# Performance work log

Hardware: AMD Instinct MI355X
Metric: run time of the kernel (lower is better)

## Reference

```python
import jax, jax.numpy as jnp
import numpy as np

B, BITS, HID = 4096, 64, 512
EPS = 1e-5
TEMPERATURE = 1.0  # buffer default


def _w(k, shape):
    return jax.random.normal(k, shape, jnp.float32) * 0.02


def setup_inputs() -> dict:
    key = jax.random.key(0)
    ks = jax.random.split(key, 8)
    return {
        "a_bits": jax.random.uniform(ks[0], (B, BITS), jnp.float32),
        "shift_bits": jax.random.uniform(ks[1], (B, BITS), jnp.float32),
        # shift_decoder params
        "W1": _w(ks[2], (HID, BITS)), "b1": jnp.zeros((HID,), jnp.float32),
        "g1": jnp.ones((HID,), jnp.float32), "be1": jnp.zeros((HID,), jnp.float32),
        "W2": _w(ks[3], (HID, HID)), "b2": jnp.zeros((HID,), jnp.float32),
        "g2": jnp.ones((HID,), jnp.float32), "be2": jnp.zeros((HID,), jnp.float32),
        "W3": _w(ks[4], (BITS, HID)), "b3": jnp.zeros((BITS,), jnp.float32),
        # index_net params (input dim = 2*BITS)
        "Wi1": _w(ks[5], (HID, 2 * BITS)), "bi1": jnp.zeros((HID,), jnp.float32),
        "Wi2": _w(ks[6], (HID, HID)), "bi2": jnp.zeros((HID,), jnp.float32),
        "Wi3": _w(ks[7], (BITS, HID)), "bi3": jnp.zeros((BITS,), jnp.float32),
    }


def _layernorm(x, g, b):
    m = jnp.mean(x, axis=-1, keepdims=True)
    v = jnp.mean(jnp.square(x - m), axis=-1, keepdims=True)
    return (x - m) * jax.lax.rsqrt(v + EPS) * g + b


def reference(a_bits, shift_bits, W1, b1, g1, be1, W2, b2, g2, be2, W3, b3,
              Wi1, bi1, Wi2, bi2, Wi3, bi3):
    # shift decoder: Linear -> LN -> ReLU -> Linear -> LN -> ReLU -> Linear
    h = jax.nn.relu(_layernorm(shift_bits @ W1.T + b1, g1, be1))
    h = jax.nn.relu(_layernorm(h @ W2.T + b2, g2, be2))
    shift_logits = h @ W3.T + b3                        # [B, BITS]
    shift_soft = jax.nn.softmax(shift_logits / TEMPERATURE, axis=-1)

    # index_net, vectorized over the output-position loop.
    # combined = [one_hot(i), shift_soft]; the one-hot part of the first Linear
    # just selects column i of Wi1[:, :BITS], so we add it as a [BITS, HID] bias.
    pos_part = Wi1[:, :BITS].T                          # [BITS, HID]
    shift_part = shift_soft @ Wi1[:, BITS:].T           # [B, HID]
    h1 = jax.nn.relu(pos_part[None, :, :] + shift_part[:, None, :] + bi1)  # [B, BITS, HID]
    h2 = jax.nn.relu(jnp.einsum('bph,kh->bpk', h1, Wi2) + bi2)             # [B, BITS, HID]
    idx_logits = jnp.einsum('bph,kh->bpk', h2, Wi3) + bi3                  # [B, BITS, BITS]
    idx_soft = jax.nn.softmax(idx_logits / TEMPERATURE, axis=-1)

    # softmax-weighted gather-sum over a_bits
    return jnp.einsum('bpj,bj->bp', idx_soft, a_bits)   # [B, BITS]
```

## Files before the change

kernel.cpp:

```cpp
#include <hip/hip_runtime.h>
#include <hip/hip_bf16.h>
#include <math.h>

#define B_N 4096
#define BITSN 64
#define HID 512
#define EPSV 1e-5f
#define BT 16

typedef unsigned short ushort_t;
typedef __attribute__((ext_vector_type(8))) short bf16x8;
typedef __attribute__((ext_vector_type(4))) float f32x4;
typedef __attribute__((ext_vector_type(16))) float f32x16;

__device__ __forceinline__ ushort_t f2bf(float f) {
  unsigned u = __float_as_uint(f);
  u += 0x7FFF + ((u >> 16) & 1);
  return (ushort_t)(u >> 16);
}

__device__ __forceinline__ unsigned pack2bf(float lo, float hi) {
  union { __hip_bfloat162 h; unsigned u; } cv;
  cv.h = __float22bfloat162_rn(make_float2(lo, hi));
  return cv.u;
}

__device__ __forceinline__ float bf2f(short v) {
  return __uint_as_float(((unsigned)(unsigned short)v) << 16);
}

__global__ __launch_bounds__(256) void prep_kernel(
    const float* __restrict__ Wi2, const float* __restrict__ Wi3,
    const float* __restrict__ Wi1, const float* __restrict__ W1,
    const float* __restrict__ W2, const float* __restrict__ W3,
    ushort_t* __restrict__ Wi1posTb, ushort_t* __restrict__ W1b,
    ushort_t* __restrict__ W2f, ushort_t* __restrict__ W3b,
    ushort_t* __restrict__ Wi1sb, ushort_t* __restrict__ Wi2f32,
    ushort_t* __restrict__ Wi3g) {
  int idx = blockIdx.x * 256 + threadIdx.x;
  if (idx < 512 * 512) {
    {
      int j = idx & 7, lane = (idx >> 3) & 63;
      int ct = (idx >> 9) & 31, ks = idx >> 14;
      int c = ct * 16 + (lane & 15);
      int k = ks * 32 + (lane >> 4) * 8 + j;
      W2f[idx] = f2bf(W2[c * 512 + k]);
    }
    {
      int j = idx & 7, lane = (idx >> 3) & 63;
      int ct = (idx >> 9) & 15, ks = idx >> 13;
      int c = ct * 32 + (lane & 31);
      int k = ks * 16 + (lane >> 5) * 8 + j;
      Wi2f32[idx] = f2bf(Wi2[c * 512 + k]);
    }
  }
  if (idx < 64 * 512) {
    W3b[idx] = f2bf(W3[idx]);
    int p = idx >> 9, i = idx & 511;
    Wi1posTb[idx] = f2bf(Wi1[i * 128 + p]);
    int e = idx & 7, lane = (idx >> 3) & 63;
    int jt = (idx >> 9) & 1, h = (idx >> 10) & 1;
    int mc = (idx >> 11) & 1, w = idx >> 12;
    int jr = jt * 32 + (lane & 31);
    int c = w * 64 + mc * 32 + 16 * h + 4 * (lane >> 5) + (e & 3) + 8 * (e >> 2);
    Wi3g[idx] = f2bf(Wi3[jr * 512 + c]);
  }
  if (idx < 512 * 64) {
    W1b[idx] = f2bf(W1[idx]);
    int j = idx >> 6, k = idx & 63;
    Wi1sb[idx] = f2bf(Wi1[j * 128 + 64 + k]);
  }
}

__global__ __launch_bounds__(256) void shift2_kernel(
    const float* __restrict__ shift_bits,
    const ushort_t* __restrict__ W1b, const float* __restrict__ b1,
    const float* __restrict__ g1, const float* __restrict__ be1,
    const ushort_t* __restrict__ W2f, const float* __restrict__ b2,
    const float* __restrict__ g2, const float* __restrict__ be2,
    const ushort_t* __restrict__ W3b, const float* __restrict__ b3,
    const ushort_t* __restrict__ Wi1sb, const float* __restrict__ bi1,
    float* __restrict__ sp) {
  __shared__ __align__(16) ushort_t hA[BT * 512];
  __shared__ __align__(16) char reg2[32 * 1024];
  __shared__ float b1s[512], g1s[512], be1s[512];
  __shared__ float b2s[512], g2s[512], be2s[512], bi1s[512];
  __shared__ float red[4][BT][2];
  __shared__ float b3s[64];

  ushort_t* sbt = (ushort_t*)reg2;
  ushort_t* h2  = (ushort_t*)reg2;
  float (*lg32)[68] = (float(*)[68])(reg2 + 16 * 1024);
  ushort_t* sb2 = (ushort_t*)(reg2 + 16 * 1024 + 16 * 68 * 4);

  int b0 = blockIdx.x * BT;
  int t = threadIdx.x, w = t >> 6, l = t & 63, lg = l >> 4, l15 = l & 15;

  b1s[t] = b1[t];  b1s[t + 256] = b1[t + 256];
  g1s[t] = g1[t];  g1s[t + 256] = g1[t + 256];
  be1s[t] = be1[t]; be1s[t + 256] = be1[t + 256];
  b2s[t] = b2[t];  b2s[t + 256] = b2[t + 256];
  g2s[t] = g2[t];  g2s[t + 256] = g2[t + 256];
  be2s[t] = be2[t]; be2s[t + 256] = be2[t + 256];
  bi1s[t] = bi1[t]; bi1s[t + 256] = bi1[t + 256];
  if (t < 64) b3s[t] = b3[t];
  if (t < 128) {
    int row = t >> 3, g = t & 7;
    const float* src = shift_bits + (size_t)(b0 + row) * 64 + g * 8;
    uint4 pk;
    pk.x = (unsigned)f2bf(src[0]) | ((unsigned)f2bf(src[1]) << 16);
    pk.y = (unsigned)f2bf(src[2]) | ((unsigned)f2bf(src[3]) << 16);
    pk.z = (unsigned)f2bf(src[4]) | ((unsigned)f2bf(src[5]) << 16);
    pk.w = (unsigned)f2bf(src[6]) | ((unsigned)f2bf(src[7]) << 16);
    *(uint4*)((char*)sbt + ((row * 128 + g * 16) ^ ((row & 7) << 4))) = pk;
  }
  __syncthreads();

  f32x4 acc[8];
#pragma unroll
  for (int nt = 0; nt < 8; ++nt) acc[nt] = (f32x4){0.f, 0.f, 0.f, 0.f};
#pragma unroll
  for (int ks = 0; ks < 2; ++ks) {
    bf16x8 af = *(const bf16x8*)((char*)sbt + ((l15 * 128 + ks * 64 + lg * 16) ^ ((l15 & 7) << 4)));
#pragma unroll
    for (int nt = 0; nt < 8; ++nt) {
      int c = w * 128 + nt * 16 + l15;
      bf16x8 bfr = *(const bf16x8*)(W1b + (size_t)c * 64 + ks * 32 + lg * 8);
      acc[nt] = __builtin_amdgcn_mfma_f32_16x16x32_bf16(af, bfr, acc[nt], 0, 0, 0);
    }
  }
  {
    float s[4] = {0.f, 0.f, 0.f, 0.f}, q[4] = {0.f, 0.f, 0.f, 0.f};
#pragma unroll
    for (int nt = 0; nt < 8; ++nt) {
      int c = w * 128 + nt * 16 + l15;
      float bb = b1s[c];
#pragma unroll
      for (int r = 0; r < 4; ++r) {
        float x = acc[nt][r] + bb;
        acc[nt][r] = x;
        s[r] += x; q[r] += x * x;
      }
    }
#pragma unroll
    for (int m = 8; m >= 1; m >>= 1)
#pragma unroll
      for (int r = 0; r < 4; ++r) { s[r] += __shfl_xor(s[r], m); q[r] += __shfl_xor(q[r], m); }
    if (l15 == 0)
#pragma unroll
      for (int r = 0; r < 4; ++r) { red[w][4 * lg + r][0] = s[r]; red[w][4 * lg + r][1] = q[r]; }
    __syncthreads();
    float mean[4], rs[4];
#pragma unroll
    for (int r = 0; r < 4; ++r) {
      int p = 4 * lg + r;
      float S = red[0][p][0] + red[1][p][0] + red[2][p][0] + red[3][p][0];
      float Q = red[0][p][1] + red[1][p][1] + red[2][p][1] + red[3][p][1];
      mean[r] = S * (1.0f / 512.0f);
      float var = Q * (1.0f / 512.0f) - mean[r] * mean[r];
      rs[r] = rsqrtf(var + EPSV);
    }
#pragma unroll
    for (int nt = 0; nt < 8; ++nt) {
      int c = w * 128 + nt * 16 + l15;
      float gg = g1s[c], bb = be1s[c];
#pragma unroll
      for (int r = 0; r < 4; ++r) {
        int p = 4 * lg + r;
        float v = (acc[nt][r] - mean[r]) * rs[r] * gg + bb;
        v = v > 0.f ? v : 0.f;
        *(ushort_t*)((char*)hA + ((p * 1024 + c * 2) ^ ((p & 7) << 4))) = f2bf(v);
      }
    }
  }
  __syncthreads();

#pragma unroll
  for (int nt = 0; nt < 8; ++nt) acc[nt] = (f32x4){0.f, 0.f, 0.f, 0.f};
  {
    const bf16x8* w2base = (const bf16x8*)W2f + ((size_t)(w * 8) * 64 + l);
#pragma unroll 2
    for (int step = 0; step < 16; ++step) {
      bf16x8 af = *(const bf16x8*)((char*)hA + ((l15 * 1024 + step * 64 + lg * 16) ^ ((l15 & 7) << 4)));
#pragma unroll
      for (int nt = 0; nt < 8; ++nt) {
        bf16x8 bfr = w2base[((size_t)step * 32 + nt) * 64];
        acc[nt] = __builtin_amdgcn_mfma_f32_16x16x32_bf16(af, bfr, acc[nt], 0, 0, 0);
      }
    }
  }
  __syncthreads();
  {
    float s[4] = {0.f, 0.f, 0.f, 0.f}, q[4] = {0.f, 0.f, 0.f, 0.f};
#pragma unroll
    for (int nt = 0; nt < 8; ++nt) {
      int c = w * 128 + nt * 16 + l15;
      float bb = b2s[c];
#pragma unroll
      for (int r = 0; r < 4; ++r) {
        float x = acc[nt][r] + bb;
        acc[nt][r] = x;
        s[r] += x; q[r] += x * x;
      }
    }
#pragma unroll
    for (int m = 8; m >= 1; m >>= 1)
#pragma unroll
      for (int r = 0; r < 4; ++r) { s[r] += __shfl_xor(s[r], m); q[r] += __shfl_xor(q[r], m); }
    if (l15 == 0)
#pragma unroll
      for (int r = 0; r < 4; ++r) { red[w][4 * lg + r][0] = s[r]; red[w][4 * lg + r][1] = q[r]; }
    __syncthreads();
    float mean[4], rs[4];
#pragma unroll
    for (int r = 0; r < 4; ++r) {
      int p = 4 * lg + r;
      float S = red[0][p][0] + red[1][p][0] + red[2][p][0] + red[3][p][0];
      float Q = red[0][p][1] + red[1][p][1] + red[2][p][1] + red[3][p][1];
      mean[r] = S * (1.0f / 512.0f);
      float var = Q * (1.0f / 512.0f) - mean[r] * mean[r];
      rs[r] = rsqrtf(var + EPSV);
    }
#pragma unroll
    for (int nt = 0; nt < 8; ++nt) {
      int c = w * 128 + nt * 16 + l15;
      float gg = g2s[c], bb = be2s[c];
#pragma unroll
      for (int r = 0; r < 4; ++r) {
        int p = 4 * lg + r;
        float v = (acc[nt][r] - mean[r]) * rs[r] * gg + bb;
        v = v > 0.f ? v : 0.f;
        *(ushort_t*)((char*)h2 + ((p * 1024 + c * 2) ^ ((p & 7) << 4))) = f2bf(v);
      }
    }
  }
  __syncthreads();

  {
    f32x4 a3 = (f32x4){0.f, 0.f, 0.f, 0.f};
#pragma unroll
    for (int ks = 0; ks < 16; ++ks) {
      bf16x8 af = *(const bf16x8*)((char*)h2 + ((l15 * 1024 + ks * 64 + lg * 16) ^ ((l15 & 7) << 4)));
      bf16x8 bfr = *(const bf16x8*)(W3b + (size_t)(w * 16 + l15) * 512 + ks * 32 + lg * 8);
      a3 = __builtin_amdgcn_mfma_f32_16x16x32_bf16(af, bfr, a3, 0, 0, 0);
    }
    int c = w * 16 + l15;
    float bb = b3s[c];
#pragma unroll
    for (int r = 0; r < 4; ++r) lg32[4 * lg + r][c] = a3[r] + bb;
  }
  __syncthreads();

  {
    int r = t >> 4, j = t & 15;
    float v[4];
    float m = -1e30f;
#pragma unroll
    for (int mq = 0; mq < 4; ++mq) { v[mq] = lg32[r][mq * 16 + j]; m = fmaxf(m, v[mq]); }
#pragma unroll
    for (int mk = 8; mk >= 1; mk >>= 1) m = fmaxf(m, __shfl_xor(m, mk));
    float ssum = 0.f;
#pragma unroll
    for (int mq = 0; mq < 4; ++mq) { v[mq] = expf(v[mq] - m); ssum += v[mq]; }
#pragma unroll
    for (int mk = 8; mk >= 1; mk >>= 1) ssum += __shfl_xor(ssum, mk);
    float inv = 1.f / ssum;
#pragma unroll
    for (int mq = 0; mq < 4; ++mq) {
      int c = mq * 16 + j;
      *(ushort_t*)((char*)sb2 + ((r * 128 + c * 2) ^ ((r & 7) << 4))) = f2bf(v[mq] * inv);
    }
  }
  __syncthreads();

  {
    f32x4 a4[8];
#pragma unroll
    for (int nt = 0; nt < 8; ++nt) a4[nt] = (f32x4){0.f, 0.f, 0.f, 0.f};
#pragma unroll
    for (int ks = 0; ks < 2; ++ks) {
      bf16x8 af = *(const bf16x8*)((char*)sb2 + ((l15 * 128 + ks * 64 + lg * 16) ^ ((l15 & 7) << 4)));
#pragma unroll
      for (int nt = 0; nt < 8; ++nt) {
        int c = w * 128 + nt * 16 + l15;
        bf16x8 bfr = *(const bf16x8*)(Wi1sb + (size_t)c * 64 + ks * 32 + lg * 8);
        a4[nt] = __builtin_amdgcn_mfma_f32_16x16x32_bf16(af, bfr, a4[nt], 0, 0, 0);
      }
    }
#pragma unroll
    for (int nt = 0; nt < 8; ++nt) {
      int c = w * 128 + nt * 16 + l15;
      float bb = bi1s[c];
#pragma unroll
      for (int r = 0; r < 4; ++r)
        sp[(size_t)(b0 + 4 * lg + r) * 512 + c] = a4[nt][r] + bb;
    }
  }
}

__global__ __launch_bounds__(512, 4) void big13_kernel(
    const float* __restrict__ a_bits, const float* __restrict__ sp,
    const ushort_t* __restrict__ posTb,
    const ushort_t* __restrict__ Wi2f32, const ushort_t* __restrict__ Wi3g,
    const float* __restrict__ bi2, const float* __restrict__ bi3,
    float* __restrict__ out) {
  __shared__ __align__(16) ushort_t h1s[36864];
  __shared__ float bi2s[512];
  __shared__ float ab[64];
  __shared__ float bi3s[64];

  int b = blockIdx.x, t = threadIdx.x;
  int w = t >> 6, l = t & 63;
  int l31 = l & 31, hi = l >> 5;

  bi2s[t] = bi2[t];
  if (t < 64) { ab[t] = a_bits[b * 64 + t]; bi3s[t] = bi3[t]; }

  {
    const float* sprow = sp + (size_t)b * 512 + l * 8;
    float4 s0 = *(const float4*)(sprow);
    float4 s1 = *(const float4*)(sprow + 4);
#pragma unroll
    for (int g = 0; g < 8; ++g) {
      int p = g * 8 + w;
      bf16x8 pr = *(const bf16x8*)(posTb + (size_t)p * 512 + l * 8);
      float v0 = fmaxf(s0.x + bf2f(pr[0]), 0.f), v1 = fmaxf(s0.y + bf2f(pr[1]), 0.f);
      float v2 = fmaxf(s0.z + bf2f(pr[2]), 0.f), v3 = fmaxf(s0.w + bf2f(pr[3]), 0.f);
      float v4 = fmaxf(s1.x + bf2f(pr[4]), 0.f), v5 = fmaxf(s1.y + bf2f(pr[5]), 0.f);
      float v6 = fmaxf(s1.z + bf2f(pr[6]), 0.f), v7 = fmaxf(s1.w + bf2f(pr[7]), 0.f);
      uint4 pk;
      pk.x = pack2bf(v0, v1); pk.y = pack2bf(v2, v3);
      pk.z = pack2bf(v4, v5); pk.w = pack2bf(v6, v7);
      *(uint4*)((char*)h1s + ((p * 1024 + l * 16) ^ ((p & 15) << 4))) = pk;
    }
  }
  __syncthreads();

  f32x16 acc[2][2];
#pragma unroll
  for (int mc = 0; mc < 2; ++mc)
#pragma unroll
    for (int np = 0; np < 2; ++np)
#pragma unroll
      for (int r = 0; r < 16; ++r) acc[mc][np][r] = 0.f;

  {
    const bf16x8* bbase = (const bf16x8*)Wi2f32 + ((size_t)(2 * w) * 64 + l);
    bf16x8 wf[4][2];
#pragma unroll
    for (int d = 0; d < 4; ++d) {
      wf[d][0] = bbase[(size_t)d * 1024];
      wf[d][1] = bbase[(size_t)d * 1024 + 64];
    }
    for (int kb = 0; kb < 8; ++kb) {
#pragma unroll
      for (int d = 0; d < 4; ++d) {
        int ks = kb * 4 + d;
        bf16x8 w0 = wf[d][0], w1 = wf[d][1];
        if (kb < 7) {
          wf[d][0] = bbase[(size_t)(ks + 4) * 1024];
          wf[d][1] = bbase[(size_t)(ks + 4) * 1024 + 64];
        }
        int row0 = l31, row1 = 32 + l31;
        bf16x8 h0 = *(const bf16x8*)((char*)h1s + ((row0 * 1024 + ks * 32 + hi * 16) ^ ((row0 & 15) << 4)));
        bf16x8 h1v = *(const bf16x8*)((char*)h1s + ((row1 * 1024 + ks * 32 + hi * 16) ^ ((row1 & 15) << 4)));
        acc[0][0] = __builtin_amdgcn_mfma_f32_32x32x16_bf16(w0, h0, acc[0][0], 0, 0, 0);
        acc[0][1] = __builtin_amdgcn_mfma_f32_32x32x16_bf16(w0, h1v, acc[0][1], 0, 0, 0);
        acc[1][0] = __builtin_amdgcn_mfma_f32_32x32x16_bf16(w1, h0, acc[1][0], 0, 0, 0);
        acc[1][1] = __builtin_amdgcn_mfma_f32_32x32x16_bf16(w1, h1v, acc[1][1], 0, 0, 0);
      }
    }
  }

  bf16x8 pkf[2][2][2];
#pragma unroll
  for (int mc = 0; mc < 2; ++mc) {
    float bia[16];
#pragma unroll
    for (int rq = 0; rq < 4; ++rq) {
      int c0 = w * 64 + mc * 32 + 8 * rq + 4 * hi;
      float4 bi4 = *(const float4*)(bi2s + c0);
      bia[4 * rq + 0] = bi4.x; bia[4 * rq + 1] = bi4.y;
      bia[4 * rq + 2] = bi4.z; bia[4 * rq + 3] = bi4.w;
    }
#pragma unroll
    for (int np = 0; np < 2; ++np) {
      float hv[16];
#pragma unroll
      for (int r = 0; r < 16; ++r) hv[r] = fmaxf(acc[mc][np][r] + bia[r], 0.f);
#pragma unroll
      for (int h = 0; h < 2; ++h) {
        unsigned d0 = pack2bf(hv[8 * h + 0], hv[8 * h + 1]);
        unsigned d1 = pack2bf(hv[8 * h + 2], hv[8 * h + 3]);
        unsigned d2 = pack2bf(hv[8 * h + 4], hv[8 * h + 5]);
        unsigned d3 = pack2bf(hv[8 * h + 6], hv[8 * h + 7]);
        union { unsigned u[4]; bf16x8 v; } cv;
        cv.u[0] = d0; cv.u[1] = d1; cv.u[2] = d2; cv.u[3] = d3;
        pkf[np][mc][h] = cv.v;
      }
    }
  }
  __syncthreads();

  f32x16 l00, l01, l10, l11;
#pragma unroll
  for (int r = 0; r < 16; ++r) { l00[r] = 0.f; l01[r] = 0.f; l10[r] = 0.f; l11[r] = 0.f; }
  {
    const bf16x8* gbase = (const bf16x8*)Wi3g + ((size_t)w * 8 * 64 + l);
#pragma unroll
    for (int mc = 0; mc < 2; ++mc) {
#pragma unroll
      for (int h = 0; h < 2; ++h) {
        bf16x8 g0 = gbase[((mc * 2 + h) * 2 + 0) * 64];
        bf16x8 g1 = gbase[((mc * 2 + h) * 2 + 1) * 64];
        l00 = __builtin_amdgcn_mfma_f32_32x32x16_bf16(pkf[0][mc][h], g0, l00, 0, 0, 0);
        l01 = __builtin_amdgcn_mfma_f32_32x32x16_bf16(pkf[0][mc][h], g1, l01, 0, 0, 0);
        l10 = __builtin_amdgcn_mfma_f32_32x32x16_bf16(pkf[1][mc][h], g0, l10, 0, 0, 0);
        l11 = __builtin_amdgcn_mfma_f32_32x32x16_bf16(pkf[1][mc][h], g1, l11, 0, 0, 0);
      }
    }
  }

  {
    unsigned* Pu = (unsigned*)h1s + (size_t)w * 2304;
#pragma unroll
    for (int r = 0; r < 16; ++r) {
      int p0 = (r & 3) + 8 * (r >> 2) + 4 * hi;
      int p1 = p0 + 32;
      Pu[p0 * 36 + l31] = pack2bf(l00[r], l01[r]);
      Pu[p1 * 36 + l31] = pack2bf(l10[r], l11[r]);
    }
  }
  __syncthreads();

  {
    int p = t >> 3, jo = t & 7;
    float slo[4] = {0.f, 0.f, 0.f, 0.f};
    float shi[4] = {0.f, 0.f, 0.f, 0.f};
#pragma unroll
    for (int wr = 0; wr < 8; ++wr) {
      const unsigned* Pu = (const unsigned*)h1s + (size_t)wr * 2304 + p * 36 + jo;
#pragma unroll
      for (int k = 0; k < 4; ++k) {
        unsigned v = Pu[8 * k];
        slo[k] += __uint_as_float(v << 16);
        shi[k] += __uint_as_float(v & 0xFFFF0000u);
      }
    }
    float s = 0.f, g = 0.f;
#pragma unroll
    for (int k = 0; k < 4; ++k) {
      int c = jo + 8 * k;
      float e0 = __expf(slo[k] + bi3s[c]);
      float e1 = __expf(shi[k] + bi3s[c + 32]);
      s += e0 + e1;
      g += e0 * ab[c] + e1 * ab[c + 32];
    }
#pragma unroll
    for (int mm = 4; mm >= 1; mm >>= 1) { s += __shfl_xor(s, mm); g += __shfl_xor(g, mm); }
    if (jo == 0) out[b * 64 + p] = g / s;
  }
}

extern "C" void kernel_launch(void* const* d_in, const int* in_sizes, int n_in,
                              void* d_out, int out_size, void* d_ws, size_t ws_size,
                              hipStream_t stream) {
  const float* a_bits     = (const float*)d_in[0];
  const float* shift_bits = (const float*)d_in[1];
  const float* W1  = (const float*)d_in[2];
  const float* b1  = (const float*)d_in[3];
  const float* g1  = (const float*)d_in[4];
  const float* be1 = (const float*)d_in[5];
  const float* W2  = (const float*)d_in[6];
  const float* b2  = (const float*)d_in[7];
  const float* g2  = (const float*)d_in[8];
  const float* be2 = (const float*)d_in[9];
  const float* W3  = (const float*)d_in[10];
  const float* b3  = (const float*)d_in[11];
  const float* Wi1 = (const float*)d_in[12];
  const float* bi1 = (const float*)d_in[13];
  const float* Wi2 = (const float*)d_in[14];
  const float* bi2 = (const float*)d_in[15];
  const float* Wi3 = (const float*)d_in[16];
  const float* bi3 = (const float*)d_in[17];
  float* out = (float*)d_out;

  float* sp = (float*)d_ws;
  ushort_t* W2f = (ushort_t*)((char*)d_ws + (size_t)B_N * HID * 4);
  ushort_t* W1b = W2f + 512 * 512;
  ushort_t* W3b = W1b + 512 * 64;
  ushort_t* Wi1sb = W3b + 64 * 512;
  ushort_t* Wi1posTb = Wi1sb + 512 * 64;
  ushort_t* Wi2f32 = Wi1posTb + 64 * 512;
  ushort_t* Wi3g = Wi2f32 + 512 * 512;

  prep_kernel<<<1024, 256, 0, stream>>>(Wi2, Wi3, Wi1, W1, W2, W3,
                                        Wi1posTb, W1b, W2f, W3b, Wi1sb, Wi2f32, Wi3g);
  shift2_kernel<<<B_N / BT, 256, 0, stream>>>(shift_bits, W1b, b1, g1, be1,
                                              W2f, b2, g2, be2, W3b, b3, Wi1sb, bi1, sp);
  big13_kernel<<<B_N, 512, 0, stream>>>(a_bits, sp, Wi1posTb, Wi2f32, Wi3g, bi2, bi3, out);
}
```

Measured before the change: 199.6 us.

## Double shift-decoder block to 512 threads with split-K final layer

The shift decoder kernel now uses 8 waves per 16-row tile instead of 4. Each wave covers 64 hidden columns, and the 64x512 output layer is split over K into two halves whose partial logits are summed during softmax. Softmax now runs on 32 lanes per row and uses the fast __expf. This is meant to raise parallelism and cut per-thread serial MFMA work in a kernel that has only 256 blocks. In exchange there are more waves per block and a wider LayerNorm reduction across 8 waves.

After: 192.7 us. 3.5% less time.

```diff
diff --git a/kernel.cpp b/kernel.cpp
--- a/kernel.cpp
+++ b/kernel.cpp
@@ -72,7 +72,7 @@
   }
 }
 
-__global__ __launch_bounds__(256) void shift2_kernel(
+__global__ __launch_bounds__(512) void shift3_kernel(
     const float* __restrict__ shift_bits,
     const ushort_t* __restrict__ W1b, const float* __restrict__ b1,
     const float* __restrict__ g1, const float* __restrict__ be1,
@@ -85,24 +85,20 @@
   __shared__ __align__(16) char reg2[32 * 1024];
   __shared__ float b1s[512], g1s[512], be1s[512];
   __shared__ float b2s[512], g2s[512], be2s[512], bi1s[512];
-  __shared__ float red[4][BT][2];
+  __shared__ float red[8][BT][2];
   __shared__ float b3s[64];
 
   ushort_t* sbt = (ushort_t*)reg2;
   ushort_t* h2  = (ushort_t*)reg2;
-  float (*lg32)[68] = (float(*)[68])(reg2 + 16 * 1024);
-  ushort_t* sb2 = (ushort_t*)(reg2 + 16 * 1024 + 16 * 68 * 4);
+  float (*lgp)[16][68] = (float(*)[16][68])(reg2 + 16 * 1024);
+  ushort_t* sb2 = (ushort_t*)(reg2 + 16 * 1024 + 2 * 16 * 68 * 4);
 
   int b0 = blockIdx.x * BT;
   int t = threadIdx.x, w = t >> 6, l = t & 63, lg = l >> 4, l15 = l & 15;
 
-  b1s[t] = b1[t];  b1s[t + 256] = b1[t + 256];
-  g1s[t] = g1[t];  g1s[t + 256] = g1[t + 256];
-  be1s[t] = be1[t]; be1s[t + 256] = be1[t + 256];
-  b2s[t] = b2[t];  b2s[t + 256] = b2[t + 256];
-  g2s[t] = g2[t];  g2s[t + 256] = g2[t + 256];
-  be2s[t] = be2[t]; be2s[t + 256] = be2[t + 256];
-  bi1s[t] = bi1[t]; bi1s[t + 256] = bi1[t + 256];
+  b1s[t] = b1[t];  g1s[t] = g1[t];  be1s[t] = be1[t];
+  b2s[t] = b2[t];  g2s[t] = g2[t];  be2s[t] = be2[t];
+  bi1s[t] = bi1[t];
   if (t < 64) b3s[t] = b3[t];
   if (t < 128) {
     int row = t >> 3, g = t & 7;
@@ -116,15 +112,15 @@
   }
   __syncthreads();
 
-  f32x4 acc[8];
-#pragma unroll
-  for (int nt = 0; nt < 8; ++nt) acc[nt] = (f32x4){0.f, 0.f, 0.f, 0.f};
+  f32x4 acc[4];
+#pragma unroll
+  for (int nt = 0; nt < 4; ++nt) acc[nt] = (f32x4){0.f, 0.f, 0.f, 0.f};
 #pragma unroll
   for (int ks = 0; ks < 2; ++ks) {
     bf16x8 af = *(const bf16x8*)((char*)sbt + ((l15 * 128 + ks * 64 + lg * 16) ^ ((l15 & 7) << 4)));
 #pragma unroll
-    for (int nt = 0; nt < 8; ++nt) {
-      int c = w * 128 + nt * 16 + l15;
+    for (int nt = 0; nt < 4; ++nt) {
+      int c = w * 64 + nt * 16 + l15;
       bf16x8 bfr = *(const bf16x8*)(W1b + (size_t)c * 64 + ks * 32 + lg * 8);
       acc[nt] = __builtin_amdgcn_mfma_f32_16x16x32_bf16(af, bfr, acc[nt], 0, 0, 0);
     }
@@ -132,8 +128,8 @@
   {
     float s[4] = {0.f, 0.f, 0.f, 0.f}, q[4] = {0.f, 0.f, 0.f, 0.f};
 #pragma unroll
-    for (int nt = 0; nt < 8; ++nt) {
-      int c = w * 128 + nt * 16 + l15;
+    for (int nt = 0; nt < 4; ++nt) {
+      int c = w * 64 + nt * 16 + l15;
       float bb = b1s[c];
 #pragma unroll
       for (int r = 0; r < 4; ++r) {
@@ -154,15 +150,16 @@
 #pragma unroll
     for (int r = 0; r < 4; ++r) {
       int p = 4 * lg + r;
-      float S = red[0][p][0] + red[1][p][0] + red[2][p][0] + red[3][p][0];
-      float Q = red[0][p][1] + red[1][p][1] + red[2][p][1] + red[3][p][1];
+      float S = 0.f, Q = 0.f;
+#pragma unroll
+      for (int ww = 0; ww < 8; ++ww) { S += red[ww][p][0]; Q += red[ww][p][1]; }
       mean[r] = S * (1.0f / 512.0f);
       float var = Q * (1.0f / 512.0f) - mean[r] * mean[r];
       rs[r] = rsqrtf(var + EPSV);
     }
 #pragma unroll
-    for (int nt = 0; nt < 8; ++nt) {
-      int c = w * 128 + nt * 16 + l15;
+    for (int nt = 0; nt < 4; ++nt) {
+      int c = w * 64 + nt * 16 + l15;
       float gg = g1s[c], bb = be1s[c];
 #pragma unroll
       for (int r = 0; r < 4; ++r) {
@@ -176,14 +173,14 @@
   __syncthreads();
 
 #pragma unroll
-  for (int nt = 0; nt < 8; ++nt) acc[nt] = (f32x4){0.f, 0.f, 0.f, 0.f};
-  {
-    const bf16x8* w2base = (const bf16x8*)W2f + ((size_t)(w * 8) * 64 + l);
+  for (int nt = 0; nt < 4; ++nt) acc[nt] = (f32x4){0.f, 0.f, 0.f, 0.f};
+  {
+    const bf16x8* w2base = (const bf16x8*)W2f + ((size_t)(w * 4) * 64 + l);
 #pragma unroll 2
     for (int step = 0; step < 16; ++step) {
       bf16x8 af = *(const bf16x8*)((char*)hA + ((l15 * 1024 + step * 64 + lg * 16) ^ ((l15 & 7) << 4)));
 #pragma unroll
-      for (int nt = 0; nt < 8; ++nt) {
+      for (int nt = 0; nt < 4; ++nt) {
         bf16x8 bfr = w2base[((size_t)step * 32 + nt) * 64];
         acc[nt] = __builtin_amdgcn_mfma_f32_16x16x32_bf16(af, bfr, acc[nt], 0, 0, 0);
       }
@@ -193,8 +190,8 @@
   {
     float s[4] = {0.f, 0.f, 0.f, 0.f}, q[4] = {0.f, 0.f, 0.f, 0.f};
 #pragma unroll
-    for (int nt = 0; nt < 8; ++nt) {
-      int c = w * 128 + nt * 16 + l15;
+    for (int nt = 0; nt < 4; ++nt) {
+      int c = w * 64 + nt * 16 + l15;
       float bb = b2s[c];
 #pragma unroll
       for (int r = 0; r < 4; ++r) {
@@ -215,15 +212,16 @@
 #pragma unroll
     for (int r = 0; r < 4; ++r) {
       int p = 4 * lg + r;
-      float S = red[0][p][0] + red[1][p][0] + red[2][p][0] + red[3][p][0];
-      float Q = red[0][p][1] + red[1][p][1] + red[2][p][1] + red[3][p][1];
+      float S = 0.f, Q = 0.f;
+#pragma unroll
+      for (int ww = 0; ww < 8; ++ww) { S += red[ww][p][0]; Q += red[ww][p][1]; }
       mean[r] = S * (1.0f / 512.0f);
       float var = Q * (1.0f / 512.0f) - mean[r] * mean[r];
       rs[r] = rsqrtf(var + EPSV);
     }
 #pragma unroll
-    for (int nt = 0; nt < 8; ++nt) {
-      int c = w * 128 + nt * 16 + l15;
+    for (int nt = 0; nt < 4; ++nt) {
+      int c = w * 64 + nt * 16 + l15;
       float gg = g2s[c], bb = be2s[c];
 #pragma unroll
       for (int r = 0; r < 4; ++r) {
@@ -237,59 +235,64 @@
   __syncthreads();
 
   {
+    int jt = w & 3, kh = w >> 2;
     f32x4 a3 = (f32x4){0.f, 0.f, 0.f, 0.f};
 #pragma unroll
-    for (int ks = 0; ks < 16; ++ks) {
+    for (int s8 = 0; s8 < 8; ++s8) {
+      int ks = kh * 8 + s8;
       bf16x8 af = *(const bf16x8*)((char*)h2 + ((l15 * 1024 + ks * 64 + lg * 16) ^ ((l15 & 7) << 4)));
-      bf16x8 bfr = *(const bf16x8*)(W3b + (size_t)(w * 16 + l15) * 512 + ks * 32 + lg * 8);
+      bf16x8 bfr = *(const bf16x8*)(W3b + (size_t)(jt * 16 + l15) * 512 + ks * 32 + lg * 8);
       a3 = __builtin_amdgcn_mfma_f32_16x16x32_bf16(af, bfr, a3, 0, 0, 0);
     }
-    int c = w * 16 + l15;
-    float bb = b3s[c];
-#pragma unroll
-    for (int r = 0; r < 4; ++r) lg32[4 * lg + r][c] = a3[r] + bb;
-  }
-  __syncthreads();
-
-  {
-    int r = t >> 4, j = t & 15;
-    float v[4];
+    int c = jt * 16 + l15;
+#pragma unroll
+    for (int r = 0; r < 4; ++r) lgp[kh][4 * lg + r][c] = a3[r];
+  }
+  __syncthreads();
+
+  {
+    int r = t >> 5, j2 = t & 31;
+    float v[2];
     float m = -1e30f;
 #pragma unroll
-    for (int mq = 0; mq < 4; ++mq) { v[mq] = lg32[r][mq * 16 + j]; m = fmaxf(m, v[mq]); }
-#pragma unroll
-    for (int mk = 8; mk >= 1; mk >>= 1) m = fmaxf(m, __shfl_xor(m, mk));
+    for (int mq = 0; mq < 2; ++mq) {
+      int c = mq * 32 + j2;
+      v[mq] = b3s[c] + lgp[0][r][c] + lgp[1][r][c];
+      m = fmaxf(m, v[mq]);
+    }
+#pragma unroll
+    for (int mk = 16; mk >= 1; mk >>= 1) m = fmaxf(m, __shfl_xor(m, mk));
     float ssum = 0.f;
 #pragma unroll
-    for (int mq = 0; mq < 4; ++mq) { v[mq] = expf(v[mq] - m); ssum += v[mq]; }
-#pragma unroll
-    for (int mk = 8; mk >= 1; mk >>= 1) ssum += __shfl_xor(ssum, mk);
+    for (int mq = 0; mq < 2; ++mq) { v[mq] = __expf(v[mq] - m); ssum += v[mq]; }
+#pragma unroll
+    for (int mk = 16; mk >= 1; mk >>= 1) ssum += __shfl_xor(ssum, mk);
     float inv = 1.f / ssum;
 #pragma unroll
-    for (int mq = 0; mq < 4; ++mq) {
-      int c = mq * 16 + j;
+    for (int mq = 0; mq < 2; ++mq) {
+      int c = mq * 32 + j2;
       *(ushort_t*)((char*)sb2 + ((r * 128 + c * 2) ^ ((r & 7) << 4))) = f2bf(v[mq] * inv);
     }
   }
   __syncthreads();
 
   {
-    f32x4 a4[8];
-#pragma unroll
-    for (int nt = 0; nt < 8; ++nt) a4[nt] = (f32x4){0.f, 0.f, 0.f, 0.f};
+    f32x4 a4[4];
+#pragma unroll
+    for (int nt = 0; nt < 4; ++nt) a4[nt] = (f32x4){0.f, 0.f, 0.f, 0.f};
 #pragma unroll
     for (int ks = 0; ks < 2; ++ks) {
       bf16x8 af = *(const bf16x8*)((char*)sb2 + ((l15 * 128 + ks * 64 + lg * 16) ^ ((l15 & 7) << 4)));
 #pragma unroll
-      for (int nt = 0; nt < 8; ++nt) {
-        int c = w * 128 + nt * 16 + l15;
+      for (int nt = 0; nt < 4; ++nt) {
+        int c = w * 64 + nt * 16 + l15;
         bf16x8 bfr = *(const bf16x8*)(Wi1sb + (size_t)c * 64 + ks * 32 + lg * 8);
         a4[nt] = __builtin_amdgcn_mfma_f32_16x16x32_bf16(af, bfr, a4[nt], 0, 0, 0);
       }
     }
 #pragma unroll
-    for (int nt = 0; nt < 8; ++nt) {
-      int c = w * 128 + nt * 16 + l15;
+    for (int nt = 0; nt < 4; ++nt) {
+      int c = w * 64 + nt * 16 + l15;
       float bb = bi1s[c];
 #pragma unroll
       for (int r = 0; r < 4; ++r)
@@ -496,7 +499,7 @@
 
   prep_kernel<<<1024, 256, 0, stream>>>(Wi2, Wi3, Wi1, W1, W2, W3,
                                         Wi1posTb, W1b, W2f, W3b, Wi1sb, Wi2f32, Wi3g);
-  shift2_kernel<<<B_N / BT, 256, 0, stream>>>(shift_bits, W1b, b1, g1, be1,
+  shift3_kernel<<<B_N / BT, 512, 0, stream>>>(shift_bits, W1b, b1, g1, be1,
                                               W2f, b2, g2, be2, W3b, b3, Wi1sb, bi1, sp);
   big13_kernel<<<B_N, 512, 0, stream>>>(a_bits, sp, Wi1posTb, Wi2f32, Wi3g, bi2, bi3, out);
 }
```
